# Kernel optimization log

Hardware: AMD Instinct MI355X
Metric: run time of the kernel (lower is better)

## Reference

```python
import jax, jax.numpy as jnp
import numpy as np

B = 131072
LATENT, COND = 32, 96
HIDDEN, OUT = 128, 64
E = 8            # num experts
NUM_LAYER = 3    # hidden layer count -> NUM_LAYER+1 expert layers
GH = 128         # gate hidden size
INPUT = LATENT + COND      # 128
INTER = LATENT + HIDDEN    # 160
EPS = 1e-5


def _u(key, shape, stdv):
    return jax.random.uniform(key, shape, jnp.float32, -stdv, stdv)


def setup_inputs() -> dict:
    key = jax.random.key(0)
    ks = jax.random.split(key, 20)
    inp = {
        'z': jax.random.normal(ks[0], (B, LATENT), jnp.float32),
        'c': jax.random.normal(ks[1], (B, COND), jnp.float32),
    }
    # expert layers: (in_dim, out_dim) per layer
    dims = [(INPUT, HIDDEN), (INTER, HIDDEN), (INTER, HIDDEN), (INTER, OUT)]
    for i, (j, k) in enumerate(dims):
        stdv = 1.0 / np.sqrt(j)
        inp[f'w{i}'] = _u(ks[2 + 2 * i], (E, j, k), stdv)
        inp[f'b{i}'] = _u(ks[3 + 2 * i], (E, k), stdv)
    # gate MLP: Linear(INPUT,GH) -> ELU -> Linear(GH,GH) -> ELU -> Linear(GH,E)
    gd = [(INPUT, GH), (GH, GH), (GH, E)]
    for i, (j, k) in enumerate(gd):
        stdv = 1.0 / np.sqrt(j)
        inp[f'gw{i}'] = _u(ks[10 + 2 * i], (j, k), stdv)
        inp[f'gb{i}'] = _u(ks[11 + 2 * i], (k,), stdv)
    return inp


def _layernorm(x):
    # F.layer_norm(x, x.shape[1:]) with no affine params
    mu = jnp.mean(x, axis=-1, keepdims=True)
    var = jnp.mean(jnp.square(x - mu), axis=-1, keepdims=True)
    return (x - mu) * jax.lax.rsqrt(var + EPS)


def reference(z, c, w0, b0, w1, b1, w2, b2, w3, b3,
              gw0, gb0, gw1, gb1, gw2, gb2):
    x = jnp.concatenate([z, c], axis=-1)                      # [B, INPUT]
    h = jax.nn.elu(x @ gw0 + gb0)
    h = jax.nn.elu(h @ gw1 + gb1)
    coeff = jax.nn.softmax(h @ gw2 + gb2, axis=-1)            # [B, E]

    layer_out = c
    layers = [(w0, b0, True), (w1, b1, True), (w2, b2, True), (w3, b3, False)]
    for w, b, act in layers:
        inp = jnp.concatenate([z, layer_out], axis=-1)        # [B, J]
        inp = _layernorm(inp)
        mixed_bias = coeff @ b                                # be,ek->bk
        mixed = jnp.einsum('be,bj,ejk->bk', coeff, inp, w)    # soft-MoE mix
        out = mixed + mixed_bias
        layer_out = jax.nn.elu(out) if act else out
    return layer_out
```

## Files before the change

### kernel.cpp

```cpp
#include <hip/hip_runtime.h>

typedef _Float16 f16;
typedef _Float16 f16x2 __attribute__((ext_vector_type(2)));
typedef _Float16 f16x4 __attribute__((ext_vector_type(4)));
typedef _Float16 f16x8 __attribute__((ext_vector_type(8)));
typedef float f32x16 __attribute__((ext_vector_type(16)));

#define DEV __device__ __forceinline__
#define MFMA16(a, b, cc) __builtin_amdgcn_mfma_f32_32x32x16_f16(a, b, cc, 0, 0, 0)


constexpr int OFF_W0 = 0;
constexpr int OFF_W1 = 131072;
constexpr int OFF_W2 = 294912;
constexpr int OFF_W3 = 458752;
constexpr int OFF_G0 = 540672;
constexpr int OFF_G1 = 557056;
constexpr int OFF_B0 = 573440;
constexpr int OFF_B1 = 575488;
constexpr int OFF_B2 = 577536;
constexpr int OFF_B3 = 579584;

__global__ __launch_bounds__(256) void repack_kernel(
    const float* __restrict__ w0, const float* __restrict__ w1,
    const float* __restrict__ w2, const float* __restrict__ w3,
    const float* __restrict__ gw0, const float* __restrict__ gw1,
    const float* __restrict__ b0, const float* __restrict__ b1,
    const float* __restrict__ b2, const float* __restrict__ b3,
    f16* __restrict__ ws)
{
  int g = blockIdx.x * 256 + threadIdx.x;
  if (g < 71680) {
    const float* src; int S, CT, K, dstoff, lg;
    if (g < 16384)      { src = w0;  S = 8;  CT = 4; K = 128; dstoff = OFF_W0; lg = g; }
    else if (g < 36864) { src = w1;  S = 10; CT = 4; K = 128; dstoff = OFF_W1; lg = g - 16384; }
    else if (g < 57344) { src = w2;  S = 10; CT = 4; K = 128; dstoff = OFF_W2; lg = g - 36864; }
    else if (g < 67584) { src = w3;  S = 10; CT = 2; K = 64;  dstoff = OFF_W3; lg = g - 57344; }
    else if (g < 69632) { src = gw0; S = 8;  CT = 4; K = 128; dstoff = OFF_G0; lg = g - 67584; }
    else                { src = gw1; S = 8;  CT = 4; K = 128; dstoff = OFF_G1; lg = g - 69632; }
    int l = lg & 63;
    int t = lg >> 6;
    int ct = t % CT; t /= CT;
    int s = t % S;
    int e = t / S;
    int J = S * 16;
    int n  = ct * 32 + (l & 31);
    int jb = s * 16 + (l >> 5) * 8;
    f16* dst = ws + dstoff + (size_t)lg * 8;
#pragma unroll
    for (int i = 0; i < 8; ++i)
      dst[i] = (f16)src[((size_t)(e * J + jb + i)) * K + n];
  } else if (g < 72576) {
    int bg = g - 71680;
    const float* src; int K, dstoff, lb;
    if (bg < 256)      { src = b0; K = 128; dstoff = OFF_B0; lb = bg; }
    else if (bg < 512) { src = b1; K = 128; dstoff = OFF_B1; lb = bg - 256; }
    else if (bg < 768) { src = b2; K = 128; dstoff = OFF_B2; lb = bg - 512; }
    else               { src = b3; K = 64;  dstoff = OFF_B3; lb = bg - 768; }
    int l = lb & 63, ct = lb >> 6;
    int n = ct * 32 + (l & 31);
    f16* dst = ws + dstoff + (size_t)lb * 8;
#pragma unroll
    for (int i = 0; i < 8; ++i)
      dst[i] = (l < 32) ? (f16)src[i * K + n] : (f16)0.0f;
  }
}

DEV unsigned char* actsp(unsigned char* acts, int row, int colb) {
  return acts + (((row << 8) + colb) ^ ((row & 15) << 4));
}

DEV f16x8 cvt8(float4 a, float4 b) {
  f16x8 r;
  r[0] = (f16)a.x; r[1] = (f16)a.y; r[2] = (f16)a.z; r[3] = (f16)a.w;
  r[4] = (f16)b.x; r[5] = (f16)b.y; r[6] = (f16)b.z; r[7] = (f16)b.w;
  return r;
}

template <int NR, int NC>
DEV void zacc(f32x16 (&a)[NR][NC]) {
#pragma unroll
  for (int rt = 0; rt < NR; ++rt)
#pragma unroll
    for (int t = 0; t < NC; ++t)
#pragma unroll
      for (int i = 0; i < 16; ++i) a[rt][t][i] = 0.f;
}

template <int NF>
DEV void rowstats(const f16x8 (&F)[NF], float invJ, float& mu, float& rs) {
  float s1 = 0.f, s2 = 0.f;
#if __has_builtin(__builtin_amdgcn_fdot2)
  const f16x2 one2 = {(f16)1.0f, (f16)1.0f};
#pragma unroll
  for (int i = 0; i < NF; ++i) {
    union { f16x8 v; f16x2 p[4]; } u;
    u.v = F[i];
#pragma unroll
    for (int q = 0; q < 4; ++q) {
      s1 = __builtin_amdgcn_fdot2(u.p[q], one2, s1, false);
      s2 = __builtin_amdgcn_fdot2(u.p[q], u.p[q], s2, false);
    }
  }
#else
#pragma unroll
  for (int i = 0; i < NF; ++i)
#pragma unroll
    for (int q = 0; q < 8; ++q) {
      float v = (float)F[i][q];
      s1 += v;
      s2 += v * v;
    }
#endif
  s1 += __shfl_xor(s1, 32, 64);
  s2 += __shfl_xor(s2, 32, 64);
  mu = s1 * invJ;
  float var = s2 * invJ - mu * mu;
  rs = rsqrtf(var + 1e-5f);
}

template <int NS, int NCTW, int CTTOT, int N16>
DEV void expert_loop(const f16x8 (&F0)[NS], const f16x8 (&F1)[NS],
                     float mu0, float rs0, float mu1, float rs1,
                     unsigned char* wb0, unsigned char* wb1,
                     const f16x8 cf0, const f16x8 cf1,
                     const f16* wsrc, const f16* nextsrc, int next_n16,
                     int ct0, int lane, int tid,
                     f32x16 (&acc)[2][NCTW]) {
#pragma unroll 2
  for (int e = 0; e < 8; ++e) {
    unsigned char* rb  = (e & 1) ? wb1 : wb0;
    unsigned char* wbn = (e & 1) ? wb0 : wb1;
    const float4* src = (const float4*)((e < 7) ? (wsrc + (size_t)(e + 1) * N16 * 8) : nextsrc);
    int n16 = (e < 7) ? N16 : next_n16;
    float4 stg[5];
#pragma unroll
    for (int k = 0; k < 5; ++k) {
      int idx = tid + k * 512;
      if (idx < n16) stg[k] = src[idx];
    }
    float p0f = rs0 * (float)cf0[e], p1f = rs1 * (float)cf1[e];
    f16 p0 = (f16)p0f, q0 = (f16)(-mu0 * p0f);
    f16 p1 = (f16)p1f, q1 = (f16)(-mu1 * p1f);
#pragma unroll
    for (int s = 0; s < NS; ++s) {
      f16x8 a0 = F0[s] * p0 + q0;
      f16x8 a1 = F1[s] * p1 + q1;
#pragma unroll
      for (int t = 0; t < NCTW; ++t) {
        f16x8 b = *(const f16x8*)(rb + (size_t)(((s * CTTOT) + (ct0 + t)) * 64 + lane) * 16);
        acc[0][t] = MFMA16(a0, b, acc[0][t]);
        acc[1][t] = MFMA16(a1, b, acc[1][t]);
      }
    }
#pragma unroll
    for (int k = 0; k < 5; ++k) {
      int idx = tid + k * 512;
      if (idx < n16) *(float4*)(wbn + (size_t)idx * 16) = stg[k];
    }
    __syncthreads();
  }
}

template <int NCTW>
DEV void bias_mfma(f32x16 (&acc)[2][NCTW], const f16x8 ca0, const f16x8 ca1,
                   const f16* pb, int ct0, int lane) {
#pragma unroll
  for (int t = 0; t < NCTW; ++t) {
    f16x8 bb = *(const f16x8*)(pb + (size_t)((ct0 + t) * 64 + lane) * 8);
    acc[0][t] = MFMA16(ca0, bb, acc[0][t]);
    acc[1][t] = MFMA16(ca1, bb, acc[1][t]);
  }
}

template <int NCTW>
DEV void store_acts(const f32x16 (&acc)[2][NCTW], unsigned char* acts,
                    int wrow, int ct0, int lr, int h) {
#pragma unroll
  for (int t = 0; t < NCTW; ++t) {
    int col = (ct0 + t) * 32 + lr;
#pragma unroll
    for (int rt = 0; rt < 2; ++rt) {
#pragma unroll
      for (int r = 0; r < 16; ++r) {
        float v = acc[rt][t][r];
        v = v > 0.f ? v : __expf(v) - 1.f;
        int rowl = (r & 3) + 8 * (r >> 2) + 4 * h;
        *(f16*)actsp(acts, wrow * 64 + rt * 32 + rowl, col * 2) = (f16)v;
      }
    }
  }
}

__global__ __launch_bounds__(512, 2) void moe_fused(
    const float* __restrict__ z, const float* __restrict__ c,
    const float* __restrict__ gb0, const float* __restrict__ gb1,
    const float* __restrict__ gw2, const float* __restrict__ gb2,
    const f16* __restrict__ ws, float* __restrict__ out)
{
  __shared__ __align__(16) unsigned char smem[151552];
  unsigned char* wb0  = smem;
  unsigned char* wb1  = smem + 40960;
  unsigned char* acts = smem + 81920;
  f16* coeffH = (f16*)(smem + 147456);

  const int tid  = threadIdx.x;
  const int lane = tid & 63;
  const int wave = tid >> 6;
  const int wrow = wave >> 1, wc = wave & 1;
  const int h = lane >> 5, lr = lane & 31;
  const int brow = blockIdx.x << 8;
  const int lrow0 = wrow * 64 + lr, lrow1 = lrow0 + 32;
  const int ct0 = wc * 2;

  {
    int row = tid >> 1, half = tid & 1;
    const float* zr = z + (size_t)(brow + row) * 32;
    const float* cr = c + (size_t)(brow + row) * 96;
#pragma unroll
    for (int jj = 0; jj < 16; ++jj) {
      int j0 = half * 64 + jj * 4;
      float4 v = (j0 < 32) ? *(const float4*)(zr + j0)
                           : *(const float4*)(cr + (j0 - 32));
      f16x4 hv = {(f16)v.x, (f16)v.y, (f16)v.z, (f16)v.w};
      *(f16x4*)actsp(acts, row, j0 * 2) = hv;
    }
  }
  float4 stgA[4];
  {
    const float4* g4 = (const float4*)(ws + OFF_G0);
#pragma unroll
    for (int k = 0; k < 4; ++k) stgA[k] = g4[tid + k * 512];
  }
  __syncthreads();

#pragma unroll
  for (int k = 0; k < 4; ++k) *(float4*)(wb0 + (size_t)(tid + k * 512) * 16) = stgA[k];
  f16x8 FX0[8], FX1[8];
#pragma unroll
  for (int s = 0; s < 8; ++s) {
    FX0[s] = *(const f16x8*)actsp(acts, lrow0, s * 32 + h * 16);
    FX1[s] = *(const f16x8*)actsp(acts, lrow1, s * 32 + h * 16);
  }
  float mu0, rs0, mu1, rs1;
  rowstats<8>(FX0, 1.f / 128.f, mu0, rs0);
  rowstats<8>(FX1, 1.f / 128.f, mu1, rs1);
  {
    const float4* g4 = (const float4*)(ws + OFF_G1);
#pragma unroll
    for (int k = 0; k < 4; ++k) stgA[k] = g4[tid + k * 512];
  }
  __syncthreads();

  f32x16 acc[2][2];
  zacc(acc);
#pragma unroll
  for (int s = 0; s < 8; ++s) {
    f16x8 b0 = *(const f16x8*)(wb0 + (size_t)((s * 4 + ct0) * 64 + lane) * 16);
    f16x8 b1 = *(const f16x8*)(wb0 + (size_t)((s * 4 + ct0 + 1) * 64 + lane) * 16);
    acc[0][0] = MFMA16(FX0[s], b0, acc[0][0]);
    acc[0][1] = MFMA16(FX0[s], b1, acc[0][1]);
    acc[1][0] = MFMA16(FX1[s], b0, acc[1][0]);
    acc[1][1] = MFMA16(FX1[s], b1, acc[1][1]);
  }
#pragma unroll
  for (int t = 0; t < 2; ++t) {
    int col = (ct0 + t) * 32 + lr;
    float bias = gb0[col];
#pragma unroll
    for (int rt = 0; rt < 2; ++rt)
#pragma unroll
      for (int r = 0; r < 16; ++r) {
        float v = acc[rt][t][r] + bias;
        v = v > 0.f ? v : __expf(v) - 1.f;
        int rowl = (r & 3) + 8 * (r >> 2) + 4 * h;
        *(f16*)actsp(acts, wrow * 64 + rt * 32 + rowl, col * 2) = (f16)v;
      }
  }
#pragma unroll
  for (int k = 0; k < 4; ++k) *(float4*)(wb1 + (size_t)(tid + k * 512) * 16) = stgA[k];
  __syncthreads();

  zacc(acc);
#pragma unroll
  for (int s = 0; s < 8; ++s) {
    f16x8 a0 = *(const f16x8*)actsp(acts, lrow0, s * 32 + h * 16);
    f16x8 a1 = *(const f16x8*)actsp(acts, lrow1, s * 32 + h * 16);
    f16x8 b0 = *(const f16x8*)(wb1 + (size_t)((s * 4 + ct0) * 64 + lane) * 16);
    f16x8 b1 = *(const f16x8*)(wb1 + (size_t)((s * 4 + ct0 + 1) * 64 + lane) * 16);
    acc[0][0] = MFMA16(a0, b0, acc[0][0]);
    acc[0][1] = MFMA16(a0, b1, acc[0][1]);
    acc[1][0] = MFMA16(a1, b0, acc[1][0]);
    acc[1][1] = MFMA16(a1, b1, acc[1][1]);
  }
  {
    const float4* g4 = (const float4*)(ws + OFF_W0);
#pragma unroll
    for (int k = 0; k < 4; ++k) stgA[k] = g4[tid + k * 512];
  }
  __syncthreads();
#pragma unroll
  for (int t = 0; t < 2; ++t) {
    int col = (ct0 + t) * 32 + lr;
    float bias = gb1[col];
#pragma unroll
    for (int rt = 0; rt < 2; ++rt)
#pragma unroll
      for (int r = 0; r < 16; ++r) {
        float v = acc[rt][t][r] + bias;
        v = v > 0.f ? v : __expf(v) - 1.f;
        int rowl = (r & 3) + 8 * (r >> 2) + 4 * h;
        *(f16*)actsp(acts, wrow * 64 + rt * 32 + rowl, col * 2) = (f16)v;
      }
  }
#pragma unroll
  for (int k = 0; k < 4; ++k) *(float4*)(wb0 + (size_t)(tid + k * 512) * 16) = stgA[k];
  __syncthreads();

  {
    int row = tid >> 1, part = tid & 1;
    float lgt[8];
#pragma unroll
    for (int e = 0; e < 8; ++e) lgt[e] = 0.f;
#pragma unroll
    for (int q = 0; q < 8; ++q) {
      f16x8 hv = *(const f16x8*)actsp(acts, row, part * 128 + q * 16);
#pragma unroll
      for (int i = 0; i < 8; ++i) {
        float hf = (float)hv[i];
        int j = part * 64 + q * 8 + i;
        const float4* gp = (const float4*)(gw2 + j * 8);
        float4 ga = gp[0], gb = gp[1];
        lgt[0] += hf * ga.x; lgt[1] += hf * ga.y; lgt[2] += hf * ga.z; lgt[3] += hf * ga.w;
        lgt[4] += hf * gb.x; lgt[5] += hf * gb.y; lgt[6] += hf * gb.z; lgt[7] += hf * gb.w;
      }
    }
#pragma unroll
    for (int e = 0; e < 8; ++e) {
      lgt[e] += __shfl_xor(lgt[e], 1, 64);
      lgt[e] += gb2[e];
    }
    float m = lgt[0];
#pragma unroll
    for (int e = 1; e < 8; ++e) m = fmaxf(m, lgt[e]);
    float ssum = 0.f, pe[8];
#pragma unroll
    for (int e = 0; e < 8; ++e) { pe[e] = __expf(lgt[e] - m); ssum += pe[e]; }
    float inv = 1.f / ssum;
    if (part == 0) {
      f16x8 ch;
#pragma unroll
      for (int e = 0; e < 8; ++e) ch[e] = (f16)(pe[e] * inv);
      *(f16x8*)(coeffH + row * 8) = ch;
    }
  }
  __syncthreads();

  const f16x8 cf0 = *(const f16x8*)(coeffH + lrow0 * 8);
  const f16x8 cf1 = *(const f16x8*)(coeffH + lrow1 * 8);

  zacc(acc);
  expert_loop<8, 2, 4, 2048>(FX0, FX1, mu0, rs0, mu1, rs1, wb0, wb1, cf0, cf1,
                             ws + OFF_W0, ws + OFF_W1, 2560,
                             ct0, lane, tid, acc);
  bias_mfma<2>(acc, cf0, cf1, ws + OFF_B0, ct0, lane);
  store_acts<2>(acc, acts, wrow, ct0, lr, h);
  __syncthreads();

  f16x8 F0[10], F1[10];
  auto load_layer_frags = [&]() {
#pragma unroll
    for (int s = 0; s < 2; ++s) {
      const float* zp0 = z + (size_t)(brow + lrow0) * 32 + s * 16 + h * 8;
      const float* zp1 = z + (size_t)(brow + lrow1) * 32 + s * 16 + h * 8;
      float4 a0 = *(const float4*)zp0, a1 = *(const float4*)(zp0 + 4);
      float4 b0_ = *(const float4*)zp1, b1_ = *(const float4*)(zp1 + 4);
      F0[s] = cvt8(a0, a1);
      F1[s] = cvt8(b0_, b1_);
    }
#pragma unroll
    for (int s = 0; s < 8; ++s) {
      F0[2 + s] = *(const f16x8*)actsp(acts, lrow0, s * 32 + h * 16);
      F1[2 + s] = *(const f16x8*)actsp(acts, lrow1, s * 32 + h * 16);
    }
    rowstats<10>(F0, 1.f / 160.f, mu0, rs0);
    rowstats<10>(F1, 1.f / 160.f, mu1, rs1);
  };

  load_layer_frags();
  zacc(acc);
  expert_loop<10, 2, 4, 2560>(F0, F1, mu0, rs0, mu1, rs1, wb0, wb1, cf0, cf1,
                              ws + OFF_W1, ws + OFF_W2, 2560,
                              ct0, lane, tid, acc);
  bias_mfma<2>(acc, cf0, cf1, ws + OFF_B1, ct0, lane);
  store_acts<2>(acc, acts, wrow, ct0, lr, h);
  __syncthreads();

  load_layer_frags();
  zacc(acc);
  expert_loop<10, 2, 4, 2560>(F0, F1, mu0, rs0, mu1, rs1, wb0, wb1, cf0, cf1,
                              ws + OFF_W2, ws + OFF_W3, 1280,
                              ct0, lane, tid, acc);
  bias_mfma<2>(acc, cf0, cf1, ws + OFF_B2, ct0, lane);
  store_acts<2>(acc, acts, wrow, ct0, lr, h);
  __syncthreads();

  load_layer_frags();
  f32x16 acc3[2][1];
  zacc(acc3);
  expert_loop<10, 1, 2, 1280>(F0, F1, mu0, rs0, mu1, rs1, wb0, wb1, cf0, cf1,
                              ws + OFF_W3, ws , 0,
                              wc, lane, tid, acc3);
  bias_mfma<1>(acc3, cf0, cf1, ws + OFF_B3, wc, lane);
  {
    int col = wc * 32 + lr;
#pragma unroll
    for (int rt = 0; rt < 2; ++rt)
#pragma unroll
      for (int r = 0; r < 16; ++r) {
        int rowl = (r & 3) + 8 * (r >> 2) + 4 * h;
        int grow = brow + wrow * 64 + rt * 32 + rowl;
        out[(size_t)grow * 64 + col] = acc3[rt][0][r];
      }
  }
}

extern "C" void kernel_launch(void* const* d_in, const int* in_sizes, int n_in,
                              void* d_out, int out_size, void* d_ws, size_t ws_size,
                              hipStream_t stream) {
  (void)in_sizes; (void)n_in; (void)out_size; (void)ws_size;
  const float* z   = (const float*)d_in[0];
  const float* c   = (const float*)d_in[1];
  const float* w0  = (const float*)d_in[2];
  const float* b0  = (const float*)d_in[3];
  const float* w1  = (const float*)d_in[4];
  const float* b1  = (const float*)d_in[5];
  const float* w2  = (const float*)d_in[6];
  const float* b2  = (const float*)d_in[7];
  const float* w3  = (const float*)d_in[8];
  const float* b3  = (const float*)d_in[9];
  const float* gw0 = (const float*)d_in[10];
  const float* gb0 = (const float*)d_in[11];
  const float* gw1 = (const float*)d_in[12];
  const float* gb1 = (const float*)d_in[13];
  const float* gw2 = (const float*)d_in[14];
  const float* gb2 = (const float*)d_in[15];
  f16* ws = (f16*)d_ws;
  float* out = (float*)d_out;

  repack_kernel<<<dim3(284), dim3(256), 0, stream>>>(
      w0, w1, w2, w3, gw0, gw1, b0, b1, b2, b3, ws);
  moe_fused<<<dim3(512), dim3(512), 0, stream>>>(
      z, c, gb0, gb1, gw2, gb2, ws, out);
}
```

Measured before the change: 442.8 us.

## Halve rows per block to 128 and use one row tile per wave

Each block now handles 128 rows instead of 256, so every wave computes a single 32-row MFMA tile rather than two, and the grid doubles to 1024 blocks. The activation region of LDS shrinks, which lowers shared memory per block and register pressure, and the expert loop is fully unrolled. The fdot2 row-statistics path is dropped in favour of the scalar loop. In exchange, each staged weight tile is reused by half as many rows, so weight traffic and synchronisation per row roughly double.

```diff
diff --git a/kernel.cpp b/kernel.cpp
--- a/kernel.cpp
+++ b/kernel.cpp
@@ -77,32 +77,9 @@
   return r;
 }
 
-template <int NR, int NC>
-DEV void zacc(f32x16 (&a)[NR][NC]) {
-#pragma unroll
-  for (int rt = 0; rt < NR; ++rt)
-#pragma unroll
-    for (int t = 0; t < NC; ++t)
-#pragma unroll
-      for (int i = 0; i < 16; ++i) a[rt][t][i] = 0.f;
-}
-
 template <int NF>
 DEV void rowstats(const f16x8 (&F)[NF], float invJ, float& mu, float& rs) {
   float s1 = 0.f, s2 = 0.f;
-#if __has_builtin(__builtin_amdgcn_fdot2)
-  const f16x2 one2 = {(f16)1.0f, (f16)1.0f};
-#pragma unroll
-  for (int i = 0; i < NF; ++i) {
-    union { f16x8 v; f16x2 p[4]; } u;
-    u.v = F[i];
-#pragma unroll
-    for (int q = 0; q < 4; ++q) {
-      s1 = __builtin_amdgcn_fdot2(u.p[q], one2, s1, false);
-      s2 = __builtin_amdgcn_fdot2(u.p[q], u.p[q], s2, false);
-    }
-  }
-#else
 #pragma unroll
   for (int i = 0; i < NF; ++i)
 #pragma unroll
@@ -111,7 +88,6 @@
       s1 += v;
       s2 += v * v;
     }
-#endif
   s1 += __shfl_xor(s1, 32, 64);
   s2 += __shfl_xor(s2, 32, 64);
   mu = s1 * invJ;
@@ -120,14 +96,13 @@
 }
 
 template <int NS, int NCTW, int CTTOT, int N16>
-DEV void expert_loop(const f16x8 (&F0)[NS], const f16x8 (&F1)[NS],
-                     float mu0, float rs0, float mu1, float rs1,
+DEV void expert_loop(const f16x8 (&F)[NS], float mu, float rs,
                      unsigned char* wb0, unsigned char* wb1,
-                     const f16x8 cf0, const f16x8 cf1,
+                     const f16x8 cf,
                      const f16* wsrc, const f16* nextsrc, int next_n16,
                      int ct0, int lane, int tid,
-                     f32x16 (&acc)[2][NCTW]) {
-#pragma unroll 2
+                     f32x16 (&acc)[NCTW]) {
+#pragma unroll
   for (int e = 0; e < 8; ++e) {
     unsigned char* rb  = (e & 1) ? wb1 : wb0;
     unsigned char* wbn = (e & 1) ? wb0 : wb1;
@@ -139,18 +114,15 @@
       int idx = tid + k * 512;
       if (idx < n16) stg[k] = src[idx];
     }
-    float p0f = rs0 * (float)cf0[e], p1f = rs1 * (float)cf1[e];
-    f16 p0 = (f16)p0f, q0 = (f16)(-mu0 * p0f);
-    f16 p1 = (f16)p1f, q1 = (f16)(-mu1 * p1f);
+    float pf = rs * (float)cf[e];
+    f16 p = (f16)pf, q = (f16)(-mu * pf);
 #pragma unroll
     for (int s = 0; s < NS; ++s) {
-      f16x8 a0 = F0[s] * p0 + q0;
-      f16x8 a1 = F1[s] * p1 + q1;
+      f16x8 a = F[s] * p + q;
 #pragma unroll
       for (int t = 0; t < NCTW; ++t) {
         f16x8 b = *(const f16x8*)(rb + (size_t)(((s * CTTOT) + (ct0 + t)) * 64 + lane) * 16);
-        acc[0][t] = MFMA16(a0, b, acc[0][t]);
-        acc[1][t] = MFMA16(a1, b, acc[1][t]);
+        acc[t] = MFMA16(a, b, acc[t]);
       }
     }
 #pragma unroll
@@ -163,31 +135,27 @@
 }
 
 template <int NCTW>
-DEV void bias_mfma(f32x16 (&acc)[2][NCTW], const f16x8 ca0, const f16x8 ca1,
-                   const f16* pb, int ct0, int lane) {
+DEV void bias_mfma(f32x16 (&acc)[NCTW], const f16x8 cf, const f16* pb,
+                   int ct0, int lane) {
 #pragma unroll
   for (int t = 0; t < NCTW; ++t) {
     f16x8 bb = *(const f16x8*)(pb + (size_t)((ct0 + t) * 64 + lane) * 8);
-    acc[0][t] = MFMA16(ca0, bb, acc[0][t]);
-    acc[1][t] = MFMA16(ca1, bb, acc[1][t]);
+    acc[t] = MFMA16(cf, bb, acc[t]);
   }
 }
 
 template <int NCTW>
-DEV void store_acts(const f32x16 (&acc)[2][NCTW], unsigned char* acts,
+DEV void store_acts(const f32x16 (&acc)[NCTW], unsigned char* acts,
                     int wrow, int ct0, int lr, int h) {
 #pragma unroll
   for (int t = 0; t < NCTW; ++t) {
     int col = (ct0 + t) * 32 + lr;
 #pragma unroll
-    for (int rt = 0; rt < 2; ++rt) {
-#pragma unroll
-      for (int r = 0; r < 16; ++r) {
-        float v = acc[rt][t][r];
-        v = v > 0.f ? v : __expf(v) - 1.f;
-        int rowl = (r & 3) + 8 * (r >> 2) + 4 * h;
-        *(f16*)actsp(acts, wrow * 64 + rt * 32 + rowl, col * 2) = (f16)v;
-      }
+    for (int r = 0; r < 16; ++r) {
+      float v = acc[t][r];
+      v = v > 0.f ? v : __expf(v) - 1.f;
+      int rowl = (r & 3) + 8 * (r >> 2) + 4 * h;
+      *(f16*)actsp(acts, wrow * 32 + rowl, col * 2) = (f16)v;
     }
   }
 }
@@ -198,28 +166,28 @@
     const float* __restrict__ gw2, const float* __restrict__ gb2,
     const f16* __restrict__ ws, float* __restrict__ out)
 {
-  __shared__ __align__(16) unsigned char smem[151552];
+  __shared__ __align__(16) unsigned char smem[116736];
   unsigned char* wb0  = smem;
   unsigned char* wb1  = smem + 40960;
   unsigned char* acts = smem + 81920;
-  f16* coeffH = (f16*)(smem + 147456);
+  f16* coeffH = (f16*)(smem + 114688);
 
   const int tid  = threadIdx.x;
   const int lane = tid & 63;
   const int wave = tid >> 6;
   const int wrow = wave >> 1, wc = wave & 1;
   const int h = lane >> 5, lr = lane & 31;
-  const int brow = blockIdx.x << 8;
-  const int lrow0 = wrow * 64 + lr, lrow1 = lrow0 + 32;
+  const int brow = blockIdx.x << 7;
+  const int lrow = wrow * 32 + lr;
   const int ct0 = wc * 2;
 
   {
-    int row = tid >> 1, half = tid & 1;
+    int row = tid >> 2, q4 = tid & 3;
     const float* zr = z + (size_t)(brow + row) * 32;
     const float* cr = c + (size_t)(brow + row) * 96;
 #pragma unroll
-    for (int jj = 0; jj < 16; ++jj) {
-      int j0 = half * 64 + jj * 4;
+    for (int jj = 0; jj < 8; ++jj) {
+      int j0 = q4 * 32 + jj * 4;
       float4 v = (j0 < 32) ? *(const float4*)(zr + j0)
                            : *(const float4*)(cr + (j0 - 32));
       f16x4 hv = {(f16)v.x, (f16)v.y, (f16)v.z, (f16)v.w};
@@ -236,15 +204,12 @@
 
 #pragma unroll
   for (int k = 0; k < 4; ++k) *(float4*)(wb0 + (size_t)(tid + k * 512) * 16) = stgA[k];
-  f16x8 FX0[8], FX1[8];
-#pragma unroll
-  for (int s = 0; s < 8; ++s) {
-    FX0[s] = *(const f16x8*)actsp(acts, lrow0, s * 32 + h * 16);
-    FX1[s] = *(const f16x8*)actsp(acts, lrow1, s * 32 + h * 16);
-  }
-  float mu0, rs0, mu1, rs1;
-  rowstats<8>(FX0, 1.f / 128.f, mu0, rs0);
-  rowstats<8>(FX1, 1.f / 128.f, mu1, rs1);
+  f16x8 FX[8];
+#pragma unroll
+  for (int s = 0; s < 8; ++s)
+    FX[s] = *(const f16x8*)actsp(acts, lrow, s * 32 + h * 16);
+  float muX, rsX;
+  rowstats<8>(FX, 1.f / 128.f, muX, rsX);
   {
     const float4* g4 = (const float4*)(ws + OFF_G1);
 #pragma unroll
@@ -252,46 +217,45 @@
   }
   __syncthreads();
 
-  f32x16 acc[2][2];
-  zacc(acc);
+  f32x16 acc[2];
+#pragma unroll
+  for (int t = 0; t < 2; ++t)
+#pragma unroll
+    for (int i = 0; i < 16; ++i) acc[t][i] = 0.f;
 #pragma unroll
   for (int s = 0; s < 8; ++s) {
     f16x8 b0 = *(const f16x8*)(wb0 + (size_t)((s * 4 + ct0) * 64 + lane) * 16);
     f16x8 b1 = *(const f16x8*)(wb0 + (size_t)((s * 4 + ct0 + 1) * 64 + lane) * 16);
-    acc[0][0] = MFMA16(FX0[s], b0, acc[0][0]);
-    acc[0][1] = MFMA16(FX0[s], b1, acc[0][1]);
-    acc[1][0] = MFMA16(FX1[s], b0, acc[1][0]);
-    acc[1][1] = MFMA16(FX1[s], b1, acc[1][1]);
+    acc[0] = MFMA16(FX[s], b0, acc[0]);
+    acc[1] = MFMA16(FX[s], b1, acc[1]);
   }
 #pragma unroll
   for (int t = 0; t < 2; ++t) {
     int col = (ct0 + t) * 32 + lr;
     float bias = gb0[col];
 #pragma unroll
-    for (int rt = 0; rt < 2; ++rt)
-#pragma unroll
-      for (int r = 0; r < 16; ++r) {
-        float v = acc[rt][t][r] + bias;
-        v = v > 0.f ? v : __expf(v) - 1.f;
-        int rowl = (r & 3) + 8 * (r >> 2) + 4 * h;
-        *(f16*)actsp(acts, wrow * 64 + rt * 32 + rowl, col * 2) = (f16)v;
-      }
+    for (int r = 0; r < 16; ++r) {
+      float v = acc[t][r] + bias;
+      v = v > 0.f ? v : __expf(v) - 1.f;
+      int rowl = (r & 3) + 8 * (r >> 2) + 4 * h;
+      *(f16*)actsp(acts, wrow * 32 + rowl, col * 2) = (f16)v;
+    }
   }
 #pragma unroll
   for (int k = 0; k < 4; ++k) *(float4*)(wb1 + (size_t)(tid + k * 512) * 16) = stgA[k];
   __syncthreads();
 
-  zacc(acc);
+#pragma unroll
+  for (int t = 0; t < 2; ++t)
+#pragma unroll
+    for (int i = 0; i < 16; ++i) acc[t][i] = 0.f;
 #pragma unroll
   for (int s = 0; s < 8; ++s) {
-    f16x8 a0 = *(const f16x8*)actsp(acts, lrow0, s * 32 + h * 16);
-    f16x8 a1 = *(const f16x8*)actsp(acts, lrow1, s * 32 + h * 16);
+    f16x8 a = *(const f16x8*)actsp(acts, lrow, s * 32 + h * 16);
     f16x8 b0 = *(const f16x8*)(wb1 + (size_t)((s * 4 + ct0) * 64 + lane) * 16);
     f16x8 b1 = *(const f16x8*)(wb1 + (size_t)((s * 4 + ct0 + 1) * 64 + lane) * 16);
-    acc[0][0] = MFMA16(a0, b0, acc[0][0]);
-    acc[0][1] = MFMA16(a0, b1, acc[0][1]);
-    acc[1][0] = MFMA16(a1, b0, acc[1][0]);
-    acc[1][1] = MFMA16(a1, b1, acc[1][1]);
+    acc[0] = MFMA16(a, b0, acc[0]);
+    acc[1] = MFMA16(a, b1, acc[1]);
   }
   {
     const float4* g4 = (const float4*)(ws + OFF_W0);
@@ -304,31 +268,29 @@
     int col = (ct0 + t) * 32 + lr;
     float bias = gb1[col];
 #pragma unroll
-    for (int rt = 0; rt < 2; ++rt)
-#pragma unroll
-      for (int r = 0; r < 16; ++r) {
-        float v = acc[rt][t][r] + bias;
-        v = v > 0.f ? v : __expf(v) - 1.f;
-        int rowl = (r & 3) + 8 * (r >> 2) + 4 * h;
-        *(f16*)actsp(acts, wrow * 64 + rt * 32 + rowl, col * 2) = (f16)v;
-      }
+    for (int r = 0; r < 16; ++r) {
+      float v = acc[t][r] + bias;
+      v = v > 0.f ? v : __expf(v) - 1.f;
+      int rowl = (r & 3) + 8 * (r >> 2) + 4 * h;
+      *(f16*)actsp(acts, wrow * 32 + rowl, col * 2) = (f16)v;
+    }
   }
 #pragma unroll
   for (int k = 0; k < 4; ++k) *(float4*)(wb0 + (size_t)(tid + k * 512) * 16) = stgA[k];
   __syncthreads();
 
   {
-    int row = tid >> 1, part = tid & 1;
+    int row = tid >> 2, part = tid & 3;
     float lgt[8];
 #pragma unroll
     for (int e = 0; e < 8; ++e) lgt[e] = 0.f;
 #pragma unroll
-    for (int q = 0; q < 8; ++q) {
-      f16x8 hv = *(const f16x8*)actsp(acts, row, part * 128 + q * 16);
+    for (int qq = 0; qq < 4; ++qq) {
+      f16x8 hv = *(const f16x8*)actsp(acts, row, part * 64 + qq * 16);
 #pragma unroll
       for (int i = 0; i < 8; ++i) {
         float hf = (float)hv[i];
-        int j = part * 64 + q * 8 + i;
+        int j = part * 32 + qq * 8 + i;
         const float4* gp = (const float4*)(gw2 + j * 8);
         float4 ga = gp[0], gb = gp[1];
         lgt[0] += hf * ga.x; lgt[1] += hf * ga.y; lgt[2] += hf * ga.z; lgt[3] += hf * ga.w;
@@ -338,6 +300,7 @@
 #pragma unroll
     for (int e = 0; e < 8; ++e) {
       lgt[e] += __shfl_xor(lgt[e], 1, 64);
+      lgt[e] += __shfl_xor(lgt[e], 2, 64);
       lgt[e] += gb2[e];
     }
     float m = lgt[0];
@@ -356,72 +319,74 @@
   }
   __syncthreads();
 
-  const f16x8 cf0 = *(const f16x8*)(coeffH + lrow0 * 8);
-  const f16x8 cf1 = *(const f16x8*)(coeffH + lrow1 * 8);
-
-  zacc(acc);
-  expert_loop<8, 2, 4, 2048>(FX0, FX1, mu0, rs0, mu1, rs1, wb0, wb1, cf0, cf1,
+  const f16x8 cf = *(const f16x8*)(coeffH + lrow * 8);
+
+#pragma unroll
+  for (int t = 0; t < 2; ++t)
+#pragma unroll
+    for (int i = 0; i < 16; ++i) acc[t][i] = 0.f;
+  expert_loop<8, 2, 4, 2048>(FX, muX, rsX, wb0, wb1, cf,
                              ws + OFF_W0, ws + OFF_W1, 2560,
                              ct0, lane, tid, acc);
-  bias_mfma<2>(acc, cf0, cf1, ws + OFF_B0, ct0, lane);
+  bias_mfma<2>(acc, cf, ws + OFF_B0, ct0, lane);
   store_acts<2>(acc, acts, wrow, ct0, lr, h);
   __syncthreads();
 
-  f16x8 F0[10], F1[10];
+  f16x8 F[10];
+  float mu, rs;
   auto load_layer_frags = [&]() {
 #pragma unroll
     for (int s = 0; s < 2; ++s) {
-      const float* zp0 = z + (size_t)(brow + lrow0) * 32 + s * 16 + h * 8;
-      const float* zp1 = z + (size_t)(brow + lrow1) * 32 + s * 16 + h * 8;
-      float4 a0 = *(const float4*)zp0, a1 = *(const float4*)(zp0 + 4);
-      float4 b0_ = *(const float4*)zp1, b1_ = *(const float4*)(zp1 + 4);
-      F0[s] = cvt8(a0, a1);
-      F1[s] = cvt8(b0_, b1_);
-    }
-#pragma unroll
-    for (int s = 0; s < 8; ++s) {
-      F0[2 + s] = *(const f16x8*)actsp(acts, lrow0, s * 32 + h * 16);
-      F1[2 + s] = *(const f16x8*)actsp(acts, lrow1, s * 32 + h * 16);
-    }
-    rowstats<10>(F0, 1.f / 160.f, mu0, rs0);
-    rowstats<10>(F1, 1.f / 160.f, mu1, rs1);
+      const float* zp = z + (size_t)(brow + lrow) * 32 + s * 16 + h * 8;
+      float4 a0 = *(const float4*)zp, a1 = *(const float4*)(zp + 4);
+      F[s] = cvt8(a0, a1);
+    }
+#pragma unroll
+    for (int s = 0; s < 8; ++s)
+      F[2 + s] = *(const f16x8*)actsp(acts, lrow, s * 32 + h * 16);
+    rowstats<10>(F, 1.f / 160.f, mu, rs);
   };
 
   load_layer_frags();
-  zacc(acc);
-  expert_loop<10, 2, 4, 2560>(F0, F1, mu0, rs0, mu1, rs1, wb0, wb1, cf0, cf1,
+#pragma unroll
+  for (int t = 0; t < 2; ++t)
+#pragma unroll
+    for (int i = 0; i < 16; ++i) acc[t][i] = 0.f;
+  expert_loop<10, 2, 4, 2560>(F, mu, rs, wb0, wb1, cf,
                               ws + OFF_W1, ws + OFF_W2, 2560,
                               ct0, lane, tid, acc);
-  bias_mfma<2>(acc, cf0, cf1, ws + OFF_B1, ct0, lane);
+  bias_mfma<2>(acc, cf, ws + OFF_B1, ct0, lane);
   store_acts<2>(acc, acts, wrow, ct0, lr, h);
   __syncthreads();
 
   load_layer_frags();
-  zacc(acc);
-  expert_loop<10, 2, 4, 2560>(F0, F1, mu0, rs0, mu1, rs1, wb0, wb1, cf0, cf1,
+#pragma unroll
+  for (int t = 0; t < 2; ++t)
+#pragma unroll
+    for (int i = 0; i < 16; ++i) acc[t][i] = 0.f;
+  expert_loop<10, 2, 4, 2560>(F, mu, rs, wb0, wb1, cf,
                               ws + OFF_W2, ws + OFF_W3, 1280,
                               ct0, lane, tid, acc);
-  bias_mfma<2>(acc, cf0, cf1, ws + OFF_B2, ct0, lane);
+  bias_mfma<2>(acc, cf, ws + OFF_B2, ct0, lane);
   store_acts<2>(acc, acts, wrow, ct0, lr, h);
   __syncthreads();
 
   load_layer_frags();
-  f32x16 acc3[2][1];
-  zacc(acc3);
-  expert_loop<10, 1, 2, 1280>(F0, F1, mu0, rs0, mu1, rs1, wb0, wb1, cf0, cf1,
+  f32x16 acc3[1];
+#pragma unroll
+  for (int i = 0; i < 16; ++i) acc3[0][i] = 0.f;
+  expert_loop<10, 1, 2, 1280>(F, mu, rs, wb0, wb1, cf,
                               ws + OFF_W3, ws , 0,
                               wc, lane, tid, acc3);
-  bias_mfma<1>(acc3, cf0, cf1, ws + OFF_B3, wc, lane);
+  bias_mfma<1>(acc3, cf, ws + OFF_B3, wc, lane);
   {
     int col = wc * 32 + lr;
 #pragma unroll
-    for (int rt = 0; rt < 2; ++rt)
-#pragma unroll
-      for (int r = 0; r < 16; ++r) {
-        int rowl = (r & 3) + 8 * (r >> 2) + 4 * h;
-        int grow = brow + wrow * 64 + rt * 32 + rowl;
-        out[(size_t)grow * 64 + col] = acc3[rt][0][r];
-      }
+    for (int r = 0; r < 16; ++r) {
+      int rowl = (r & 3) + 8 * (r >> 2) + 4 * h;
+      int grow = brow + wrow * 32 + rowl;
+      out[(size_t)grow * 64 + col] = acc3[0][r];
+    }
   }
 }
 
@@ -450,6 +415,6 @@
 
   repack_kernel<<<dim3(284), dim3(256), 0, stream>>>(
       w0, w1, w2, w3, gw0, gw1, b0, b1, b2, b3, ws);
-  moe_fused<<<dim3(512), dim3(512), 0, stream>>>(
+  moe_fused<<<dim3(1024), dim3(512), 0, stream>>>(
       z, c, gb0, gb1, gw2, gb2, ws, out);
 }
```

Measured after the change: 501.0 us. 13.1% more time.
